# Kernel optimization log

Hardware: AMD Instinct MI355X
Metric: run time of the kernel (lower is better)

The kernel has to match this reference:

```python
import jax, jax.numpy as jnp
import numpy as np

B, F, NB, E = 32768, 64, 64, 32


def setup_inputs() -> dict:
    key = jax.random.key(0)
    k1, k2, k3, k4 = jax.random.split(key, 4)
    x = jax.random.normal(k1, (B, F), dtype=jnp.float32)
    # per-feature sorted bin edges (as produced by PLE.adapt quantiles)
    bins = jnp.sort(jax.random.uniform(k2, (F, NB), dtype=jnp.float32,
                                       minval=-2.0, maxval=2.0), axis=1)
    W = jax.random.normal(k3, (F, NB, E), dtype=jnp.float32) / np.sqrt(NB)
    b = jax.random.normal(k4, (F, E), dtype=jnp.float32)
    return {"x": x, "bins": bins, "W": W, "b": b}


def reference(x, bins, W, b):
    # x: [B,F], bins: [F,NB] sorted edges, W: [F,NB,E], b: [F,E]
    nb = bins.shape[1]
    lo = bins  # bins[j] == lookup_table[i-1] for bin i=j+1
    # lookup_table.get(i, -1): last bin has no upper edge -> defaults to -1.0
    hi = jnp.concatenate(
        [bins[:, 1:], jnp.full((bins.shape[0], 1), -1.0, bins.dtype)], axis=1)
    j = jnp.arange(nb)
    xe = x[:, :, None]                                  # [B,F,1]
    left = (xe < lo[None]) & (j > 0)                    # [B,F,NB]
    right = (xe >= hi[None]) & (j < nb - 1)             # [B,F,NB]
    v = (xe - lo[None]) / (hi - lo)[None]               # interpolation value
    # enc = 0 where left, 1 where neither, v where exactly one of left/right
    enc = jnp.where(left != right, v, jnp.where(left, 0.0, 1.0))  # [B,F,NB]
    # per-feature linear + ReLU, then features stacked along dim 1
    emb = jax.nn.relu(jnp.einsum('bfn,fne->bfe', enc, W) + b[None])  # [B,F,E]
    return emb
```

## Files before the change

### kernel.cpp

```cpp
#include <hip/hip_runtime.h>


#define FDIM 64
#define NB   64
#define EDIM 32

typedef __attribute__((ext_vector_type(4))) float f32x4;
typedef __attribute__((ext_vector_type(4))) int   i32x4;

__global__ __launch_bounds__(256) void prep_kernel(
    const float* __restrict__ bins, const float* __restrict__ W,
    const float* __restrict__ bias,
    float* __restrict__ P, float* __restrict__ R)
{
    const int f = blockIdx.x;
    const int t = threadIdx.x;
    __shared__ float sg[NB];
    __shared__ float sb[NB];
    __shared__ float redP[8][EDIM];
    __shared__ float redQ[8][EDIM];

    if (t < NB) {
        float lo = bins[f * NB + t];
        float hi = (t < NB - 1) ? bins[f * NB + t + 1] : -1.0f;
        sg[t] = 1.0f / (hi - lo);
        sb[t] = lo;
    }
    __syncthreads();

    const int e  = t & (EDIM - 1);
    const int ch = t >> 5;
    float p = 0.0f, q = 0.0f;
    const float* Wf = W + (size_t)f * NB * EDIM + e;
    #pragma unroll
    for (int i = 0; i < 8; ++i) {
        int n = ch * 8 + i;
        float w = Wf[n * EDIM];
        p = fmaf(sg[n], w, p);
        q = fmaf(sb[n] * sg[n], w, q);
    }
    redP[ch][e] = p;
    redQ[ch][e] = q;
    __syncthreads();

    if (t < EDIM) {
        float P_ = 0.0f, Q_ = 0.0f;
        #pragma unroll
        for (int c = 0; c < 8; ++c) { P_ += redP[c][t]; Q_ += redQ[c][t]; }
        P[f * EDIM + t] = P_;
        R[f * EDIM + t] = bias[f * EDIM + t] - Q_;
    }
}

__global__ __launch_bounds__(256) void nemb_kernel(
    const float* __restrict__ x, const float* __restrict__ bins,
    const float* __restrict__ W,
    const float* __restrict__ P, const float* __restrict__ R,
    float* __restrict__ out)
{
    __shared__ float sBins[FDIM * (NB + 1)];
    __shared__ float sX[16 * 64];
    __shared__ float sC[16 * 64];
    __shared__ int   sK[16 * 64];

    const int t = threadIdx.x;

    #pragma unroll
    for (int i = 0; i < 4; ++i) {
        int li = i * 256 + t;
        f32x4 v = reinterpret_cast<const f32x4*>(bins)[li];
        int el = li * 4;
        int f = el >> 6, n = el & 63;
        float* d = &sBins[f * (NB + 1) + n];
        d[0] = v.x; d[1] = v.y; d[2] = v.z; d[3] = v.w;
    }
    if (t < FDIM) sBins[t * (NB + 1) + NB] = -1.0f;
    __syncthreads();

    const int w  = t >> 6;
    const int l  = t & 63;
    const int u  = l >> 4;
    const int m  = l & 15;
    const int d8 = l >> 3;
    const int e0 = (l & 7) * 4;
    const long g = (long)blockIdx.x * 4 + w;
    const int prow = w * 4;

    f32x4 x4 = __builtin_nontemporal_load(
        reinterpret_cast<const f32x4*>(x + (4 * g + u) * FDIM + 4 * m));

    float cc[4]; int kk[4];
    #pragma unroll
    for (int j = 0; j < 4; ++j) {
        const float* bl = &sBins[(4 * m + j) * (NB + 1)];
        float xv = x4[j];
        int k = (bl[32] <= xv) ? 32 : 0;
        if (bl[k + 16] <= xv) k += 16;
        if (bl[k +  8] <= xv) k +=  8;
        if (bl[k +  4] <= xv) k +=  4;
        if (bl[k +  2] <= xv) k +=  2;
        if (bl[k +  1] <= xv) k +=  1;
        float lo = bl[k];
        float hi = bl[k + 1];
        cc[j] = (hi - xv) * __builtin_amdgcn_rcpf(hi - lo);
        kk[j] = k;
    }

    {
        int wbase = (prow + u) * 64 + ((4 * m + 8 * u) & 63);
        *reinterpret_cast<f32x4*>(&sX[wbase]) = x4;
        f32x4 cv4; cv4.x = cc[0]; cv4.y = cc[1]; cv4.z = cc[2]; cv4.w = cc[3];
        *reinterpret_cast<f32x4*>(&sC[wbase]) = cv4;
        i32x4 kv4; kv4.x = kk[0]; kv4.y = kk[1]; kv4.z = kk[2]; kv4.w = kk[3];
        *reinterpret_cast<i32x4*>(&sK[wbase]) = kv4;
    }
    asm volatile("s_waitcnt lgkmcnt(0)" ::: "memory");

    float* og = out + (4 * g) * (FDIM * EDIM);
    #pragma unroll
    for (int i = 0; i < 8; ++i) {
        const int fi = 8 * i + d8;
        f32x4 Pv = *reinterpret_cast<const f32x4*>(P + fi * EDIM + e0);
        f32x4 Rv = *reinterpret_cast<const f32x4*>(R + fi * EDIM + e0);
        #pragma unroll
        for (int r = 0; r < 4; ++r) {
            int idx = (prow + r) * 64 + ((fi + 8 * r) & 63);
            float xv = sX[idx];
            float cv = sC[idx];
            int   kv = sK[idx];
            f32x4 Wv = *reinterpret_cast<const f32x4*>(
                W + ((fi * NB + kv) * EDIM) + e0);
            f32x4 o;
            o.x = fmaxf(fmaf(cv, Wv.x, fmaf(xv, Pv.x, Rv.x)), 0.0f);
            o.y = fmaxf(fmaf(cv, Wv.y, fmaf(xv, Pv.y, Rv.y)), 0.0f);
            o.z = fmaxf(fmaf(cv, Wv.z, fmaf(xv, Pv.z, Rv.z)), 0.0f);
            o.w = fmaxf(fmaf(cv, Wv.w, fmaf(xv, Pv.w, Rv.w)), 0.0f);
            *reinterpret_cast<f32x4*>(og + (long)r * (FDIM * EDIM)
                                      + fi * EDIM + e0) = o;
        }
    }
}

extern "C" void kernel_launch(void* const* d_in, const int* in_sizes, int n_in,
                              void* d_out, int out_size, void* d_ws, size_t ws_size,
                              hipStream_t stream) {
    const float* x    = (const float*)d_in[0];
    const float* bins = (const float*)d_in[1];
    const float* W    = (const float*)d_in[2];
    const float* bias = (const float*)d_in[3];
    float* out = (float*)d_out;

    float* P = (float*)d_ws;
    float* R = P + FDIM * EDIM;

    const int B = in_sizes[0] / FDIM;

    prep_kernel<<<FDIM, 256, 0, stream>>>(bins, W, bias, P, R);
    nemb_kernel<<<B / 16, 256, 0, stream>>>(x, bins, W, P, R, out);
}
```

Measured before the change: 62.10 us.

## Split features into slices and stage W slice in LDS per block

Each block now handles 8 features for 256 rows instead of all 64 features for 16 rows. It copies that feature slice of W (64 KB, padded) into shared memory, so the per-row gathers of W read from LDS instead of global memory or L2. The block loops over the rows in 32-row steps, reusing the staged W and bins. The cost is a large shared-memory footprint per block, which limits occupancy. Output stores now write 8-feature strips per row instead of contiguous full rows, and the x loads become scalar, strided reads.

```diff
diff --git a/kernel.cpp b/kernel.cpp
--- a/kernel.cpp
+++ b/kernel.cpp
@@ -4,9 +4,11 @@
 #define FDIM 64
 #define NB   64
 #define EDIM 32
+#define FSL  8
+#define NRPB 256
+#define WPAD 33
 
 typedef __attribute__((ext_vector_type(4))) float f32x4;
-typedef __attribute__((ext_vector_type(4))) int   i32x4;
 
 __global__ __launch_bounds__(256) void prep_kernel(
     const float* __restrict__ bins, const float* __restrict__ W,
@@ -58,42 +60,56 @@
     const float* __restrict__ P, const float* __restrict__ R,
     float* __restrict__ out)
 {
-    __shared__ float sBins[FDIM * (NB + 1)];
-    __shared__ float sX[16 * 64];
-    __shared__ float sC[16 * 64];
-    __shared__ int   sK[16 * 64];
+    __shared__ float sW[FSL * NB * WPAD];
+    __shared__ float sBins[FSL * 65];
+    __shared__ float pX[4][64];
+    __shared__ float pC[4][64];
+    __shared__ int   pK[4][64];
 
-    const int t = threadIdx.x;
+    const int t     = threadIdx.x;
+    const int slice = blockIdx.x & 7;
+    const int chunk = blockIdx.x >> 3;
+    const int f0    = slice * FSL;
 
+    const float* Wg = W + (size_t)f0 * NB * EDIM;
     #pragma unroll
-    for (int i = 0; i < 4; ++i) {
-        int li = i * 256 + t;
-        f32x4 v = reinterpret_cast<const f32x4*>(bins)[li];
-        int el = li * 4;
-        int f = el >> 6, n = el & 63;
-        float* d = &sBins[f * (NB + 1) + n];
+    for (int i = 0; i < 16; ++i) {
+        int qi = i * 256 + t;
+        f32x4 v = reinterpret_cast<const f32x4*>(Wg)[qi];
+        int gi = qi * 4;
+        int fl = gi >> 11;
+        int n  = (gi >> 5) & 63;
+        int e0 = gi & 31;
+        *reinterpret_cast<f32x4*>(&sW[fl * (NB * WPAD) + n * WPAD + e0]) = v;
+    }
+    if (t < 128) {
+        f32x4 v = reinterpret_cast<const f32x4*>(bins + f0 * NB)[t];
+        int gi = t * 4;
+        int fl = gi >> 6, n = gi & 63;
+        float* d = &sBins[fl * 65 + n];
         d[0] = v.x; d[1] = v.y; d[2] = v.z; d[3] = v.w;
     }
-    if (t < FDIM) sBins[t * (NB + 1) + NB] = -1.0f;
+    if (t < FSL) sBins[t * 65 + 64] = -1.0f;
     __syncthreads();
 
     const int w  = t >> 6;
     const int l  = t & 63;
-    const int u  = l >> 4;
-    const int m  = l & 15;
-    const int d8 = l >> 3;
+    const int rs = l >> 3;
+    const int fs = l & 7;
+    const int ft = l >> 3;
     const int e0 = (l & 7) * 4;
-    const long g = (long)blockIdx.x * 4 + w;
-    const int prow = w * 4;
 
-    f32x4 x4 = __builtin_nontemporal_load(
-        reinterpret_cast<const f32x4*>(x + (4 * g + u) * FDIM + 4 * m));
+    const f32x4 Pv = *reinterpret_cast<const f32x4*>(P + (f0 + ft) * EDIM + e0);
+    const f32x4 Rv = *reinterpret_cast<const f32x4*>(R + (f0 + ft) * EDIM + e0);
 
-    float cc[4]; int kk[4];
-    #pragma unroll
-    for (int j = 0; j < 4; ++j) {
-        const float* bl = &sBins[(4 * m + j) * (NB + 1)];
-        float xv = x4[j];
+    const long r00 = (long)chunk * NRPB;
+
+    #pragma unroll 2
+    for (int it = 0; it < NRPB / 32; ++it) {
+        const long rb = r00 + it * 32 + w * 8;
+
+        float xv = x[(rb + rs) * FDIM + f0 + fs];
+        const float* bl = &sBins[fs * 65];
         int k = (bl[32] <= xv) ? 32 : 0;
         if (bl[k + 16] <= xv) k += 16;
         if (bl[k +  8] <= xv) k +=  8;
@@ -102,41 +118,27 @@
         if (bl[k +  1] <= xv) k +=  1;
         float lo = bl[k];
         float hi = bl[k + 1];
-        cc[j] = (hi - xv) * __builtin_amdgcn_rcpf(hi - lo);
-        kk[j] = k;
-    }
+        float cv = (hi - xv) * __builtin_amdgcn_rcpf(hi - lo);
 
-    {
-        int wbase = (prow + u) * 64 + ((4 * m + 8 * u) & 63);
-        *reinterpret_cast<f32x4*>(&sX[wbase]) = x4;
-        f32x4 cv4; cv4.x = cc[0]; cv4.y = cc[1]; cv4.z = cc[2]; cv4.w = cc[3];
-        *reinterpret_cast<f32x4*>(&sC[wbase]) = cv4;
-        i32x4 kv4; kv4.x = kk[0]; kv4.y = kk[1]; kv4.z = kk[2]; kv4.w = kk[3];
-        *reinterpret_cast<i32x4*>(&sK[wbase]) = kv4;
-    }
-    asm volatile("s_waitcnt lgkmcnt(0)" ::: "memory");
+        pX[w][rs * 8 + fs] = xv;
+        pC[w][rs * 8 + fs] = cv;
+        pK[w][rs * 8 + fs] = k;
+        asm volatile("s_waitcnt lgkmcnt(0)" ::: "memory");
 
-    float* og = out + (4 * g) * (FDIM * EDIM);
-    #pragma unroll
-    for (int i = 0; i < 8; ++i) {
-        const int fi = 8 * i + d8;
-        f32x4 Pv = *reinterpret_cast<const f32x4*>(P + fi * EDIM + e0);
-        f32x4 Rv = *reinterpret_cast<const f32x4*>(R + fi * EDIM + e0);
         #pragma unroll
-        for (int r = 0; r < 4; ++r) {
-            int idx = (prow + r) * 64 + ((fi + 8 * r) & 63);
-            float xv = sX[idx];
-            float cv = sC[idx];
-            int   kv = sK[idx];
+        for (int r = 0; r < 8; ++r) {
+            float xr = pX[w][r * 8 + ft];
+            float cr = pC[w][r * 8 + ft];
+            int   kr = pK[w][r * 8 + ft];
             f32x4 Wv = *reinterpret_cast<const f32x4*>(
-                W + ((fi * NB + kv) * EDIM) + e0);
+                &sW[ft * (NB * WPAD) + kr * WPAD + e0]);
             f32x4 o;
-            o.x = fmaxf(fmaf(cv, Wv.x, fmaf(xv, Pv.x, Rv.x)), 0.0f);
-            o.y = fmaxf(fmaf(cv, Wv.y, fmaf(xv, Pv.y, Rv.y)), 0.0f);
-            o.z = fmaxf(fmaf(cv, Wv.z, fmaf(xv, Pv.z, Rv.z)), 0.0f);
-            o.w = fmaxf(fmaf(cv, Wv.w, fmaf(xv, Pv.w, Rv.w)), 0.0f);
-            *reinterpret_cast<f32x4*>(og + (long)r * (FDIM * EDIM)
-                                      + fi * EDIM + e0) = o;
+            o.x = fmaxf(fmaf(cr, Wv.x, fmaf(xr, Pv.x, Rv.x)), 0.0f);
+            o.y = fmaxf(fmaf(cr, Wv.y, fmaf(xr, Pv.y, Rv.y)), 0.0f);
+            o.z = fmaxf(fmaf(cr, Wv.z, fmaf(xr, Pv.z, Rv.z)), 0.0f);
+            o.w = fmaxf(fmaf(cr, Wv.w, fmaf(xr, Pv.w, Rv.w)), 0.0f);
+            *reinterpret_cast<f32x4*>(
+                out + (rb + r) * (FDIM * EDIM) + (f0 + ft) * EDIM + e0) = o;
         }
     }
 }
@@ -154,7 +156,8 @@
     float* R = P + FDIM * EDIM;
 
     const int B = in_sizes[0] / FDIM;
+    const int nchunks = B / NRPB;
 
     prep_kernel<<<FDIM, 256, 0, stream>>>(bins, W, bias, P, R);
-    nemb_kernel<<<B / 16, 256, 0, stream>>>(x, bins, W, P, R, out);
+    nemb_kernel<<<nchunks * 8, 256, 0, stream>>>(x, bins, W, P, R, out);
 }
```

After: 59.35 us. 4.4% less time.
